# Optimization experiments

Measured on AMD Instinct MI355X. Metric: run time of the kernel, lower is better.

The kernel has to match this reference:

```python
import jax, jax.numpy as jnp
import numpy as np

VOCAB, EMB, HID, NCLS = 50257, 48, 128, 2000
B, S = 512, 1024


def setup_inputs() -> dict:
    key = jax.random.key(0)
    ks = jax.random.split(key, 8)
    x = jax.random.randint(ks[0], (B, S), 0, VOCAB)
    emb_table = jax.random.normal(ks[1], (VOCAB, EMB), dtype=jnp.float32)
    emb_table = emb_table.at[0].set(0.0)  # padding_idx=0
    k_ih = 1.0 / np.sqrt(HID)
    w_ih = jax.random.uniform(ks[2], (4 * HID, EMB), minval=-k_ih, maxval=k_ih, dtype=jnp.float32)
    w_hh = jax.random.uniform(ks[3], (4 * HID, HID), minval=-k_ih, maxval=k_ih, dtype=jnp.float32)
    b_ih = jax.random.uniform(ks[4], (4 * HID,), minval=-k_ih, maxval=k_ih, dtype=jnp.float32)
    b_hh = jax.random.uniform(ks[5], (4 * HID,), minval=-k_ih, maxval=k_ih, dtype=jnp.float32)
    k_fc = 1.0 / np.sqrt(HID)
    w_fc = jax.random.uniform(ks[6], (NCLS, HID), minval=-k_fc, maxval=k_fc, dtype=jnp.float32)
    b_fc = jax.random.uniform(ks[7], (NCLS,), minval=-k_fc, maxval=k_fc, dtype=jnp.float32)
    return {"x": x, "emb_table": emb_table, "w_ih": w_ih, "w_hh": w_hh,
            "b_ih": b_ih, "b_hh": b_hh, "w_fc": w_fc, "b_fc": b_fc}


def _lstm_last_hidden(e, w_ih, w_hh, b_ih, b_hh):
    # e: [B, S, E]. Precompute input contributions for all timesteps (one big GEMM).
    xg = jnp.einsum('bse,ge->bsg', e, w_ih) + b_ih + b_hh  # [B, S, 4H]
    xg = jnp.transpose(xg, (1, 0, 2))                      # [S, B, 4H]
    Bn = e.shape[0]
    h0 = jnp.zeros((Bn, HID), e.dtype)
    c0 = jnp.zeros((Bn, HID), e.dtype)

    def step(carry, xg_t):
        h, c = carry
        g = xg_t + h @ w_hh.T                              # [B, 4H]
        i, f, gg, o = jnp.split(g, 4, axis=-1)             # PyTorch gate order i,f,g,o
        i = jax.nn.sigmoid(i)
        f = jax.nn.sigmoid(f)
        gg = jnp.tanh(gg)
        o = jax.nn.sigmoid(o)
        c = f * c + i * gg
        h = o * jnp.tanh(c)
        return (h, c), None

    (h_n, _), _ = jax.lax.scan(step, (h0, c0), xg)
    return h_n


def reference(x, emb_table, w_ih, w_hh, b_ih, b_hh, w_fc, b_fc):
    e = emb_table[x]                                       # [B, S, E] gather
    h_n = _lstm_last_hidden(e, w_ih, w_hh, b_ih, b_hh)     # [B, H]
    return h_n @ w_fc.T + b_fc                             # [B, NCLS]
```

## Files before the change

### kernel.cpp

```cpp
#include <hip/hip_runtime.h>

#define DI __device__ __forceinline__

typedef unsigned int uint;
typedef unsigned short ushort;
typedef _Float16 half2t __attribute__((ext_vector_type(2)));
typedef _Float16 f16x8 __attribute__((ext_vector_type(8)));
typedef float f32x4 __attribute__((ext_vector_type(4)));

#define VOCAB 50257
#define NEMB 48
#define HID 128
#define G4 512
#define NCLS 2000
#define BATCH 512
#define SEQ 1024
#define MROWS 2
#define NBLK2 (BATCH / MROWS)

DI float sigm(float x) {
  return __builtin_amdgcn_rcpf(1.0f + __builtin_amdgcn_exp2f(-1.4426950408889634f * x));
}
DI float tanhfast(float x) {
  return 1.0f - 2.0f * __builtin_amdgcn_rcpf(__builtin_amdgcn_exp2f(2.8853900817779268f * x) + 1.0f);
}

DI void barrier_lds_only() {
  asm volatile("s_waitcnt lgkmcnt(0)" ::: "memory");
  __builtin_amdgcn_s_barrier();
  asm volatile("" ::: "memory");
}

#define VROWS 32
__global__ __launch_bounds__(512) void build_P(
    const float* __restrict__ emb, const float* __restrict__ w_ih,
    const float* __restrict__ b_ih, const float* __restrict__ b_hh,
    _Float16* __restrict__ P)
{
  __shared__ __align__(16) float eL[VROWS][NEMB];
  const int tid = threadIdx.x;
  const int v0 = blockIdx.x * VROWS;
  int nrows = VOCAB - v0; if (nrows > VROWS) nrows = VROWS;

  for (int f = tid; f < nrows * NEMB; f += 512)
    eL[f / NEMB][f % NEMB] = emb[(size_t)v0 * NEMB + f];

  float w[NEMB];
  {
    const float* wr = w_ih + (size_t)tid * NEMB;
#pragma unroll
    for (int k = 0; k < NEMB; k++) w[k] = wr[k];
  }
  float bias = b_ih[tid] + b_hh[tid];
  const int pidx = ((tid & 127) << 2) + (tid >> 7);
  __syncthreads();

  for (int v = 0; v < nrows; v++) {
    const float4* e4 = (const float4*)&eL[v][0];
    float a = bias;
#pragma unroll
    for (int k = 0; k < NEMB / 4; k++) {
      float4 e = e4[k];
      a += w[4 * k] * e.x + w[4 * k + 1] * e.y + w[4 * k + 2] * e.z + w[4 * k + 3] * e.w;
    }
    P[(size_t)(v0 + v) * G4 + pidx] = (_Float16)a;
  }
}

__global__ __launch_bounds__(512, 2) void lstm_mfma4(
    const int* __restrict__ x, const float* __restrict__ w_hh,
    const _Float16* __restrict__ P, float* __restrict__ hout)
{
  __shared__ ushort tokL[MROWS][SEQ];
  __shared__ __align__(16) _Float16 hbuf[2][16][HID];

  const int tid  = threadIdx.x;
  const int lane = tid & 63;
  const int wave = tid >> 6;
  const int l15  = lane & 15;
  const int lg   = lane >> 4;
  const int u    = wave * 16 + l15;
  const int blk  = blockIdx.x;

  {
    const int* xp = x + (size_t)blk * MROWS * SEQ;
    for (int i = tid; i < MROWS * SEQ; i += 512) ((ushort*)tokL)[i] = (ushort)xp[i];
  }
  {
    uint4 z; z.x = z.y = z.z = z.w = 0u;
    ((uint4*)hbuf)[tid] = z;
  }

  f16x8 Bf[4][4];
#pragma unroll
  for (int g = 0; g < 4; g++) {
    const float* wr = w_hh + (size_t)(g * 128 + u) * HID + lg * 8;
#pragma unroll
    for (int ck = 0; ck < 4; ck++) {
      const float4* p4 = (const float4*)(wr + ck * 32);
      float4 wa = p4[0], wb = p4[1];
      f16x8 f;
      f[0] = (_Float16)wa.x; f[1] = (_Float16)wa.y;
      f[2] = (_Float16)wa.z; f[3] = (_Float16)wa.w;
      f[4] = (_Float16)wb.x; f[5] = (_Float16)wb.y;
      f[6] = (_Float16)wb.z; f[7] = (_Float16)wb.w;
      Bf[g][ck] = f;
    }
  }

  int aoff[4];
#pragma unroll
  for (int ck = 0; ck < 4; ck++)
    aoff[ck] = l15 * 256 + ((((ck * 4 + lg) ^ l15)) << 4);

  const int hwoff0 = u * 2;
  const int hwoff1 = 256 + ((((u >> 3) ^ 1)) << 4) + (u & 7) * 2;
  float cst0 = 0.0f, cst1 = 0.0f;

  __syncthreads();

  uint2 xgA0 = {0,0}, xgA1 = {0,0}, xgB0 = {0,0}, xgB1 = {0,0};
  if (lg == 0) {
    xgA0 = *(const uint2*)(P + (size_t)tokL[0][0] * G4 + u * 4);
    xgA1 = *(const uint2*)(P + (size_t)tokL[1][0] * G4 + u * 4);
    xgB0 = *(const uint2*)(P + (size_t)tokL[0][1] * G4 + u * 4);
    xgB1 = *(const uint2*)(P + (size_t)tokL[1][1] * G4 + u * 4);
  }

  const f32x4 fz = {0.f, 0.f, 0.f, 0.f};
  const char* hB = (const char*)hbuf;
  char* hW = (char*)hbuf;

#define MF(Areg, ckk, a0, a1, a2, a3) do {                                     \
    a0 = __builtin_amdgcn_mfma_f32_16x16x32_f16(Areg, Bf[0][ckk], a0, 0, 0, 0);\
    a1 = __builtin_amdgcn_mfma_f32_16x16x32_f16(Areg, Bf[1][ckk], a1, 0, 0, 0);\
    a2 = __builtin_amdgcn_mfma_f32_16x16x32_f16(Areg, Bf[2][ckk], a2, 0, 0, 0);\
    a3 = __builtin_amdgcn_mfma_f32_16x16x32_f16(Areg, Bf[3][ckk], a3, 0, 0, 0);\
  } while (0)

#define STEP(t, par) do {                                                      \
    const char* hc = hB + (par) * 4096;                                        \
    f16x8 A0 = *(const f16x8*)(hc + aoff[0]);                                  \
    f16x8 A1 = *(const f16x8*)(hc + aoff[1]);                                  \
    f16x8 A2 = *(const f16x8*)(hc + aoff[2]);                                  \
    f16x8 A3 = *(const f16x8*)(hc + aoff[3]);                                  \
    f32x4 a0 = fz, a1 = fz, a2 = fz, a3 = fz;                                  \
    MF(A0, 0, a0, a1, a2, a3);                                                 \
    MF(A1, 1, a0, a1, a2, a3);                                                 \
    MF(A2, 2, a0, a1, a2, a3);                                                 \
    MF(A3, 3, a0, a1, a2, a3);                                                 \
    if (lg == 0) {                                                             \
      uint2 xc0 = (par) ? xgB0 : xgA0;           \
      uint2 xc1 = (par) ? xgB1 : xgA1;                                         \
      int tc = (t) + 2; if (tc > SEQ - 1) tc = SEQ - 1;                        \
      int tk0 = tokL[0][tc], tk1 = tokL[1][tc];                                \
      uint2 v0 = *(const uint2*)(P + (size_t)tk0 * G4 + u * 4);                \
      uint2 v1 = *(const uint2*)(P + (size_t)tk1 * G4 + u * 4);                \
      if (par) { xgB0 = v0; xgB1 = v1; } else { xgA0 = v0; xgA1 = v1; }        \
      char* hn = hW + ((par) ^ 1) * 4096;                                      \
                                                    \
      {                                                                        \
        half2t x0 = __builtin_bit_cast(half2t, xc0.x);                         \
        half2t x1 = __builtin_bit_cast(half2t, xc0.y);                         \
        float gi = a0[0] + (float)x0.x;                                        \
        float gf = a1[0] + (float)x0.y;                                        \
        float gc = a2[0] + (float)x1.x;                                        \
        float go = a3[0] + (float)x1.y;                                        \
        float fi = sigm(gi), ff = sigm(gf), gt = tanhfast(gc), fo = sigm(go);  \
        cst0 = ff * cst0 + fi * gt;                                            \
        float hh = fo * tanhfast(cst0);                                        \
        *(_Float16*)(hn + hwoff0) = (_Float16)hh;                              \
        if ((t) == SEQ - 1)                                                    \
          hout[((size_t)blk * MROWS + 0) * HID + u] = hh;                      \
      }                                                                        \
                                                    \
      {                                                                        \
        half2t x0 = __builtin_bit_cast(half2t, xc1.x);                         \
        half2t x1 = __builtin_bit_cast(half2t, xc1.y);                         \
        float gi = a0[1] + (float)x0.x;                                        \
        float gf = a1[1] + (float)x0.y;                                        \
        float gc = a2[1] + (float)x1.x;                                        \
        float go = a3[1] + (float)x1.y;                                        \
        float fi = sigm(gi), ff = sigm(gf), gt = tanhfast(gc), fo = sigm(go);  \
        cst1 = ff * cst1 + fi * gt;                                            \
        float hh = fo * tanhfast(cst1);                                        \
        *(_Float16*)(hn + hwoff1) = (_Float16)hh;                              \
        if ((t) == SEQ - 1)                                                    \
          hout[((size_t)blk * MROWS + 1) * HID + u] = hh;                      \
      }                                                                        \
    }                                                                          \
    barrier_lds_only();                                                        \
  } while (0)

  for (int t = 0; t < SEQ; t += 2) { STEP(t, 0); STEP(t + 1, 1); }
#undef STEP
#undef MF
}

typedef _Float16 h2 __attribute__((ext_vector_type(2)));
DI float fdot2f(h2 a, h2 b, float c) { return c + (float)a.x * (float)b.x + (float)a.y * (float)b.y; }

__global__ __launch_bounds__(512, 4) void lstm_scan_fb(
    const int* __restrict__ x, const float* __restrict__ emb,
    const float* __restrict__ w_ih, const float* __restrict__ w_hh,
    const float* __restrict__ b_ih, const float* __restrict__ b_hh,
    float* __restrict__ hout)
{
  __shared__ int tokL[SEQ];
  __shared__ __align__(16) _Float16 h16[HID];
  __shared__ float g2h[2][G4];
  __shared__ __align__(8) h2 e16[2][NEMB / 2];

  const int tid = threadIdx.x;
  const int b = blockIdx.x;
  const int col = tid & 255;
  const int kh = tid >> 8;
  const int koff = kh * (HID / 2);

  {
    const int* xp = x + (size_t)b * SEQ;
#pragma unroll
    for (int i = 0; i < SEQ / 512; i++) tokL[tid + 512 * i] = xp[tid + 512 * i];
  }

  h2 w0[HID / 4], w1[HID / 4];
  {
    const float4* wr0 = (const float4*)(w_hh + (size_t)col * HID + koff);
    const float4* wr1 = (const float4*)(w_hh + (size_t)(col + 256) * HID + koff);
#pragma unroll
    for (int k = 0; k < HID / 8; k++) {
      float4 a = wr0[k];
      h2 p; p.x = (_Float16)a.x; p.y = (_Float16)a.y; w0[2 * k] = p;
      p.x = (_Float16)a.z; p.y = (_Float16)a.w; w0[2 * k + 1] = p;
      float4 bv = wr1[k];
      p.x = (_Float16)bv.x; p.y = (_Float16)bv.y; w1[2 * k] = p;
      p.x = (_Float16)bv.z; p.y = (_Float16)bv.w; w1[2 * k + 1] = p;
    }
  }
  h2 wih0[NEMB / 2], wih1[NEMB / 2];
  float bias0 = 0.0f, bias1 = 0.0f;
  if (kh == 0) {
    const float* wr0 = w_ih + (size_t)col * NEMB;
    const float* wr1 = w_ih + (size_t)(col + 256) * NEMB;
#pragma unroll
    for (int k = 0; k < NEMB / 2; k++) {
      h2 p;
      p.x = (_Float16)wr0[2 * k]; p.y = (_Float16)wr0[2 * k + 1]; wih0[k] = p;
      p.x = (_Float16)wr1[2 * k]; p.y = (_Float16)wr1[2 * k + 1]; wih1[k] = p;
    }
    bias0 = b_ih[col] + b_hh[col];
    bias1 = b_ih[col + 256] + b_hh[col + 256];
  }
  if (tid < HID) h16[tid] = (_Float16)0.0f;
  __syncthreads();

  float c = 0.0f;
  float2 einfl = {0.0f, 0.0f};
  if (tid < NEMB / 2) {
    float2 e0 = ((const float2*)(emb + (size_t)tokL[0] * NEMB))[tid];
    einfl    = ((const float2*)(emb + (size_t)tokL[1] * NEMB))[tid];
    h2 p; p.x = (_Float16)e0.x; p.y = (_Float16)e0.y;
    e16[0][tid] = p;
  }
  __syncthreads();

#define STEPF(t, par) do {                                                     \
    float xg0, xg1;                                                            \
    if (tid < NEMB / 2) {                                                      \
      int tc = (t) + 2; if (tc > SEQ - 1) tc = SEQ - 1;                        \
      h2 p; p.x = (_Float16)einfl.x; p.y = (_Float16)einfl.y;                  \
      e16[((t) + 1) & 1][tid] = p;                                             \
      einfl = ((const float2*)(emb + (size_t)tokL[tc] * NEMB))[tid];           \
    }                                                                          \
    if (kh == 0) {                                                             \
      xg0 = bias0; xg1 = bias1;                                                \
      _Pragma("unroll")                                                        \
      for (int k = 0; k < NEMB / 2; k++) {                                     \
        xg0 = fdot2f(wih0[k], e16[(par)][k], xg0);                             \
        xg1 = fdot2f(wih1[k], e16[(par)][k], xg1);                             \
      }                                                                        \
    } else { xg0 = 0.0f; xg1 = 0.0f; }                                         \
    const uint4* hv = (const uint4*)h16 + (kh << 3);                           \
    float s0 = xg0, u0 = 0.0f, s1 = xg1, u1 = 0.0f;                            \
    _Pragma("unroll")                                                          \
    for (int kt = 0; kt < HID / 16; kt++) {                                    \
      uint4 hq = hv[kt];                                                       \
      h2 ha = __builtin_bit_cast(h2, hq.x);                                    \
      h2 hb = __builtin_bit_cast(h2, hq.y);                                    \
      h2 hc = __builtin_bit_cast(h2, hq.z);                                    \
      h2 hd = __builtin_bit_cast(h2, hq.w);                                    \
      s0 = fdot2f(w0[4 * kt + 0], ha, s0);                                     \
      u0 = fdot2f(w0[4 * kt + 1], hb, u0);                                     \
      s0 = fdot2f(w0[4 * kt + 2], hc, s0);                                     \
      u0 = fdot2f(w0[4 * kt + 3], hd, u0);                                     \
      s1 = fdot2f(w1[4 * kt + 0], ha, s1);                                     \
      u1 = fdot2f(w1[4 * kt + 1], hb, u1);                                     \
      s1 = fdot2f(w1[4 * kt + 2], hc, s1);                                     \
      u1 = fdot2f(w1[4 * kt + 3], hd, u1);                                     \
    }                                                                          \
    g2h[kh][col] = s0 + u0;                                                    \
    g2h[kh][col + 256] = s1 + u1;                                              \
    barrier_lds_only();                                                        \
    if (tid < HID) {                                                           \
      float gi = g2h[0][tid]           + g2h[1][tid];                          \
      float gf = g2h[0][HID + tid]     + g2h[1][HID + tid];                    \
      float gc = g2h[0][2 * HID + tid] + g2h[1][2 * HID + tid];                \
      float go = g2h[0][3 * HID + tid] + g2h[1][3 * HID + tid];                \
      float fi = sigm(gi), ff = sigm(gf), gt = tanhfast(gc), fo = sigm(go);    \
      c = ff * c + fi * gt;                                                    \
      float hh = fo * tanhfast(c);                                             \
      h16[tid] = (_Float16)hh;                                                 \
      if ((t) == SEQ - 1) hout[(size_t)b * HID + tid] = hh;                    \
    }                                                                          \
    barrier_lds_only();                                                        \
  } while (0)

  for (int t = 0; t < SEQ; t += 2) { STEPF(t, 0); STEPF(t + 1, 1); }
#undef STEPF
}

#define FCR 64
#define FCC 64
__global__ __launch_bounds__(256) void fc_kernel(
    const float* __restrict__ h, const float* __restrict__ w_fc,
    const float* __restrict__ b_fc, float* __restrict__ out)
{
  __shared__ float aT[HID][FCR];
  __shared__ float bT[HID][FCC];
  const int tid = threadIdx.x;
  const int r0 = blockIdx.y * FCR;
  const int c0 = blockIdx.x * FCC;

  for (int f = tid; f < FCR * (HID / 4); f += 256) {
    int row = f >> 5, q = f & 31;
    float4 v = ((const float4*)h)[(((size_t)(r0 + row)) << 5) + q];
    aT[4 * q + 0][row] = v.x; aT[4 * q + 1][row] = v.y;
    aT[4 * q + 2][row] = v.z; aT[4 * q + 3][row] = v.w;
    int wrow = c0 + row;
    float4 wv;
    if (wrow < NCLS) wv = ((const float4*)w_fc)[(((size_t)wrow) << 5) + q];
    else { wv.x = 0.f; wv.y = 0.f; wv.z = 0.f; wv.w = 0.f; }
    bT[4 * q + 0][row] = wv.x; bT[4 * q + 1][row] = wv.y;
    bT[4 * q + 2][row] = wv.z; bT[4 * q + 3][row] = wv.w;
  }
  __syncthreads();

  const int cr = tid & 15, rr = tid >> 4;
  float acc[4][4];
#pragma unroll
  for (int i = 0; i < 4; i++)
#pragma unroll
    for (int j = 0; j < 4; j++) acc[i][j] = 0.0f;

#pragma unroll 4
  for (int k = 0; k < HID; k++) {
    float4 av = *(const float4*)&aT[k][4 * rr];
    float4 bv = *(const float4*)&bT[k][4 * cr];
    float a[4] = {av.x, av.y, av.z, av.w};
    float bb[4] = {bv.x, bv.y, bv.z, bv.w};
#pragma unroll
    for (int i = 0; i < 4; i++)
#pragma unroll
      for (int j = 0; j < 4; j++) acc[i][j] += a[i] * bb[j];
  }

#pragma unroll
  for (int j = 0; j < 4; j++) {
    int cc = c0 + 4 * cr + j;
    if (cc < NCLS) {
      float bias = b_fc[cc];
#pragma unroll
      for (int i = 0; i < 4; i++)
        out[(size_t)(r0 + 4 * rr + i) * NCLS + cc] = acc[i][j] + bias;
    }
  }
}

extern "C" void kernel_launch(void* const* d_in, const int* in_sizes, int n_in,
                              void* d_out, int out_size, void* d_ws, size_t ws_size,
                              hipStream_t stream) {
  const int*   xx   = (const int*)d_in[0];
  const float* emb  = (const float*)d_in[1];
  const float* w_ih = (const float*)d_in[2];
  const float* w_hh = (const float*)d_in[3];
  const float* b_ih = (const float*)d_in[4];
  const float* b_hh = (const float*)d_in[5];
  const float* w_fc = (const float*)d_in[6];
  const float* b_fc = (const float*)d_in[7];
  float* out = (float*)d_out;

  const size_t pbytes = (size_t)VOCAB * G4 * sizeof(_Float16);
  const size_t palign = (pbytes + 255) & ~(size_t)255;
  const size_t hbytes = (size_t)BATCH * HID * sizeof(float);

  float* hout;
  if (ws_size >= palign + hbytes) {
    _Float16* P = (_Float16*)d_ws;
    hout = (float*)((char*)d_ws + palign);
    build_P<<<(VOCAB + VROWS - 1) / VROWS, 512, 0, stream>>>(emb, w_ih, b_ih, b_hh, P);
    lstm_mfma4<<<NBLK2, 512, 0, stream>>>(xx, w_hh, P, hout);
  } else {
    hout = (float*)d_ws;
    lstm_scan_fb<<<BATCH, 512, 0, stream>>>(xx, emb, w_ih, w_hh, b_ih, b_hh, hout);
  }
  dim3 fcg((NCLS + FCC - 1) / FCC, BATCH / FCR);
  fc_kernel<<<fcg, 256, 0, stream>>>(hout, w_fc, b_fc, out);
}
```

Baseline: 869.0 us.

## Process one batch row per block and launch one block per sequence

Each LSTM block now handles a single batch row instead of two, launching 512 blocks instead of 256, with launch bounds raised to allow four blocks per CU. This spreads the serial recurrence across more CUs and waves, cutting per-step gate work per thread, but the MFMA now uses only one of its 16 A rows, so tensor-core work per useful row doubles. Register pressure must also fit the higher occupancy target.

```diff
diff --git a/kernel.cpp b/kernel.cpp
--- a/kernel.cpp
+++ b/kernel.cpp
@@ -15,8 +15,6 @@
 #define NCLS 2000
 #define BATCH 512
 #define SEQ 1024
-#define MROWS 2
-#define NBLK2 (BATCH / MROWS)
 
 DI float sigm(float x) {
   return __builtin_amdgcn_rcpf(1.0f + __builtin_amdgcn_exp2f(-1.4426950408889634f * x));
@@ -67,11 +65,11 @@
   }
 }
 
-__global__ __launch_bounds__(512, 2) void lstm_mfma4(
+__global__ __launch_bounds__(512, 4) void lstm_mfma5(
     const int* __restrict__ x, const float* __restrict__ w_hh,
     const _Float16* __restrict__ P, float* __restrict__ hout)
 {
-  __shared__ ushort tokL[MROWS][SEQ];
+  __shared__ ushort tokL[SEQ];
   __shared__ __align__(16) _Float16 hbuf[2][16][HID];
 
   const int tid  = threadIdx.x;
@@ -83,8 +81,9 @@
   const int blk  = blockIdx.x;
 
   {
-    const int* xp = x + (size_t)blk * MROWS * SEQ;
-    for (int i = tid; i < MROWS * SEQ; i += 512) ((ushort*)tokL)[i] = (ushort)xp[i];
+    const int* xp = x + (size_t)blk * SEQ;
+#pragma unroll
+    for (int i = 0; i < SEQ / 512; i++) tokL[tid + 512 * i] = (ushort)xp[tid + 512 * i];
   }
   {
     uint4 z; z.x = z.y = z.z = z.w = 0u;
@@ -114,17 +113,14 @@
     aoff[ck] = l15 * 256 + ((((ck * 4 + lg) ^ l15)) << 4);
 
   const int hwoff0 = u * 2;
-  const int hwoff1 = 256 + ((((u >> 3) ^ 1)) << 4) + (u & 7) * 2;
-  float cst0 = 0.0f, cst1 = 0.0f;
-
-  __syncthreads();
-
-  uint2 xgA0 = {0,0}, xgA1 = {0,0}, xgB0 = {0,0}, xgB1 = {0,0};
+  float cst0 = 0.0f;
+
+  __syncthreads();
+
+  uint2 xgA0 = {0, 0}, xgB0 = {0, 0};
   if (lg == 0) {
-    xgA0 = *(const uint2*)(P + (size_t)tokL[0][0] * G4 + u * 4);
-    xgA1 = *(const uint2*)(P + (size_t)tokL[1][0] * G4 + u * 4);
-    xgB0 = *(const uint2*)(P + (size_t)tokL[0][1] * G4 + u * 4);
-    xgB1 = *(const uint2*)(P + (size_t)tokL[1][1] * G4 + u * 4);
+    xgA0 = *(const uint2*)(P + (size_t)tokL[0] * G4 + u * 4);
+    xgB0 = *(const uint2*)(P + (size_t)tokL[1] * G4 + u * 4);
   }
 
   const f32x4 fz = {0.f, 0.f, 0.f, 0.f};
@@ -151,43 +147,23 @@
     MF(A3, 3, a0, a1, a2, a3);                                                 \
     if (lg == 0) {                                                             \
       uint2 xc0 = (par) ? xgB0 : xgA0;           \
-      uint2 xc1 = (par) ? xgB1 : xgA1;                                         \
       int tc = (t) + 2; if (tc > SEQ - 1) tc = SEQ - 1;                        \
-      int tk0 = tokL[0][tc], tk1 = tokL[1][tc];                                \
+      int tk0 = tokL[tc];                                                      \
       uint2 v0 = *(const uint2*)(P + (size_t)tk0 * G4 + u * 4);                \
-      uint2 v1 = *(const uint2*)(P + (size_t)tk1 * G4 + u * 4);                \
-      if (par) { xgB0 = v0; xgB1 = v1; } else { xgA0 = v0; xgA1 = v1; }        \
+      if (par) xgB0 = v0; else xgA0 = v0;                                      \
       char* hn = hW + ((par) ^ 1) * 4096;                                      \
-                                                    \
-      {                                                                        \
-        half2t x0 = __builtin_bit_cast(half2t, xc0.x);                         \
-        half2t x1 = __builtin_bit_cast(half2t, xc0.y);                         \
-        float gi = a0[0] + (float)x0.x;                                        \
-        float gf = a1[0] + (float)x0.y;                                        \
-        float gc = a2[0] + (float)x1.x;                                        \
-        float go = a3[0] + (float)x1.y;                                        \
-        float fi = sigm(gi), ff = sigm(gf), gt = tanhfast(gc), fo = sigm(go);  \
-        cst0 = ff * cst0 + fi * gt;                                            \
-        float hh = fo * tanhfast(cst0);                                        \
-        *(_Float16*)(hn + hwoff0) = (_Float16)hh;                              \
-        if ((t) == SEQ - 1)                                                    \
-          hout[((size_t)blk * MROWS + 0) * HID + u] = hh;                      \
-      }                                                                        \
-                                                    \
-      {                                                                        \
-        half2t x0 = __builtin_bit_cast(half2t, xc1.x);                         \
-        half2t x1 = __builtin_bit_cast(half2t, xc1.y);                         \
-        float gi = a0[1] + (float)x0.x;                                        \
-        float gf = a1[1] + (float)x0.y;                                        \
-        float gc = a2[1] + (float)x1.x;                                        \
-        float go = a3[1] + (float)x1.y;                                        \
-        float fi = sigm(gi), ff = sigm(gf), gt = tanhfast(gc), fo = sigm(go);  \
-        cst1 = ff * cst1 + fi * gt;                                            \
-        float hh = fo * tanhfast(cst1);                                        \
-        *(_Float16*)(hn + hwoff1) = (_Float16)hh;                              \
-        if ((t) == SEQ - 1)                                                    \
-          hout[((size_t)blk * MROWS + 1) * HID + u] = hh;                      \
-      }                                                                        \
+      half2t x0 = __builtin_bit_cast(half2t, xc0.x);                           \
+      half2t x1 = __builtin_bit_cast(half2t, xc0.y);                           \
+      float gi = a0[0] + (float)x0.x;                                          \
+      float gf = a1[0] + (float)x0.y;                                          \
+      float gc = a2[0] + (float)x1.x;                                          \
+      float go = a3[0] + (float)x1.y;                                          \
+      float fi = sigm(gi), ff = sigm(gf), gt = tanhfast(gc), fo = sigm(go);    \
+      cst0 = ff * cst0 + fi * gt;                                              \
+      float hh = fo * tanhfast(cst0);                                          \
+      *(_Float16*)(hn + hwoff0) = (_Float16)hh;                                \
+      if ((t) == SEQ - 1)                                                      \
+        hout[(size_t)blk * HID + u] = hh;                                      \
     }                                                                          \
     barrier_lds_only();                                                        \
   } while (0)
@@ -398,7 +374,7 @@
     _Float16* P = (_Float16*)d_ws;
     hout = (float*)((char*)d_ws + palign);
     build_P<<<(VOCAB + VROWS - 1) / VROWS, 512, 0, stream>>>(emb, w_ih, b_ih, b_hh, P);
-    lstm_mfma4<<<NBLK2, 512, 0, stream>>>(xx, w_hh, P, hout);
+    lstm_mfma5<<<BATCH, 512, 0, stream>>>(xx, w_hh, P, hout);
   } else {
     hout = (float*)d_ws;
     lstm_scan_fb<<<BATCH, 512, 0, stream>>>(xx, emb, w_ih, w_hh, b_ih, b_hh, hout);
```

Result: slower. 965.4 us (+11.1%).
